# Performance work log

Hardware: AMD Instinct MI355X
Metric: run time of the kernel (lower is better)

## Reference

```python
import jax, jax.numpy as jnp
import numpy as np

D = 1024
H = 16
HD = D // H
FF = 4096
EPS = 1e-5


def setup_inputs() -> dict:
    key = jax.random.key(0)
    ks = jax.random.split(key, 12)
    s = lambda fan_in: 1.0 / np.sqrt(fan_in)
    return {
        "x": jax.random.normal(ks[0], (8, 1024, D), dtype=jnp.float32),
        "ln1_g": jnp.ones((D,), jnp.float32),
        "ln1_b": jnp.zeros((D,), jnp.float32),
        "ln2_g": jnp.ones((D,), jnp.float32),
        "ln2_b": jnp.zeros((D,), jnp.float32),
        "qkv_w": jax.random.uniform(ks[1], (3 * D, D), jnp.float32, -s(D), s(D)),
        "q_bias": jnp.zeros((D,), jnp.float32),
        "v_bias": jnp.zeros((D,), jnp.float32),
        "proj_w": jax.random.uniform(ks[2], (D, D), jnp.float32, -s(D), s(D)),
        "proj_b": jnp.zeros((D,), jnp.float32),
        "fc1_w": jax.random.uniform(ks[3], (FF, D), jnp.float32, -s(D), s(D)),
        "fc1_b": jnp.zeros((FF,), jnp.float32),
        "fc2_w": jax.random.uniform(ks[4], (D, FF), jnp.float32, -s(FF), s(FF)),
        "fc2_b": jnp.zeros((D,), jnp.float32),
    }


def _layernorm(x, g, b):
    mu = jnp.mean(x, axis=-1, keepdims=True)
    var = jnp.mean(jnp.square(x - mu), axis=-1, keepdims=True)
    return (x - mu) * jax.lax.rsqrt(var + EPS) * g + b


def reference(x, ln1_g, ln1_b, ln2_g, ln2_b, qkv_w, q_bias, v_bias,
              proj_w, proj_b, fc1_w, fc1_b, fc2_w, fc2_b):
    b, n, d = x.shape
    scale = HD ** (-0.5)
    # --- attention branch ---
    h = _layernorm(x, ln1_g, ln1_b)
    qkv_bias = jnp.concatenate([q_bias, jnp.zeros_like(v_bias), v_bias])
    qkv = h @ qkv_w.T + qkv_bias  # [b, n, 3d]
    qkv = qkv.reshape(b, n, 3, H, HD).transpose(2, 0, 3, 1, 4)  # [3, b, h, n, hd]
    q, k, v = qkv[0], qkv[1], qkv[2]
    attn = jnp.einsum("bhnd,bhmd->bhnm", q * scale, k)
    attn = jax.nn.softmax(attn, axis=-1)
    o = jnp.einsum("bhnm,bhmd->bhnd", attn, v)
    o = o.transpose(0, 2, 1, 3).reshape(b, n, d)
    x = x + (o @ proj_w.T + proj_b)
    # --- mlp branch ---
    h = _layernorm(x, ln2_g, ln2_b)
    h = jax.nn.gelu(h @ fc1_w.T + fc1_b, approximate=False)
    x = x + (h @ fc2_w.T + fc2_b)
    return x
```

## Files before the change

### kernel.cpp

```cpp
#include <hip/hip_runtime.h>
#include <hip/hip_bf16.h>


typedef __attribute__((ext_vector_type(8))) short short8;
typedef __attribute__((ext_vector_type(4))) float floatx4;

__device__ __forceinline__ unsigned short f2bf(float f) {
  union { __hip_bfloat16 h; unsigned short u; } cv;
  cv.h = __float2bfloat16(f);
  return cv.u;
}

__device__ __forceinline__ float fast_exp2(float x) {
  return __builtin_amdgcn_exp2f(x);
}

__device__ __forceinline__ void async_ld16(const void* g, void* l) {
  __builtin_amdgcn_global_load_lds(
      (const __attribute__((address_space(1))) unsigned int*)g,
      (__attribute__((address_space(3))) unsigned int*)l, 16, 0, 0);
}

#define VMCNT(n) asm volatile("s_waitcnt vmcnt(" #n ")" ::: "memory")

__global__ __launch_bounds__(256) void cvt_bf16(const float* __restrict__ in,
                                                unsigned short* __restrict__ out) {
  const long i = ((long)blockIdx.x * 256 + threadIdx.x) * 4;
  const float4 v = *(const float4*)(in + i);
  ushort4 o;
  o.x = f2bf(v.x); o.y = f2bf(v.y); o.z = f2bf(v.z); o.w = f2bf(v.w);
  *(ushort4*)(out + i) = o;
}

__global__ __launch_bounds__(256) void ln_bf16(const float* __restrict__ x,
                                               const float* __restrict__ g,
                                               const float* __restrict__ b,
                                               unsigned short* __restrict__ out) {
  const int row = blockIdx.x;
  const int tid = threadIdx.x;
  const float4 v = ((const float4*)(x + (long)row * 1024))[tid];
  float s = v.x + v.y + v.z + v.w;
  float ss = v.x * v.x + v.y * v.y + v.z * v.z + v.w * v.w;
#pragma unroll
  for (int off = 1; off < 64; off <<= 1) {
    s += __shfl_xor(s, off);
    ss += __shfl_xor(ss, off);
  }
  __shared__ float red[8];
  const int wave = tid >> 6, lane = tid & 63;
  if (lane == 0) { red[wave] = s; red[4 + wave] = ss; }
  __syncthreads();
  if (tid == 0) {
    red[0] = red[0] + red[1] + red[2] + red[3];
    red[4] = red[4] + red[5] + red[6] + red[7];
  }
  __syncthreads();
  const float mu = red[0] * (1.f / 1024.f);
  const float var = red[4] * (1.f / 1024.f) - mu * mu;
  const float rstd = rsqrtf(var + 1e-5f);
  const int c = tid * 4;
  ushort4 o;
  o.x = f2bf((v.x - mu) * rstd * g[c + 0] + b[c + 0]);
  o.y = f2bf((v.y - mu) * rstd * g[c + 1] + b[c + 1]);
  o.z = f2bf((v.z - mu) * rstd * g[c + 2] + b[c + 2]);
  o.w = f2bf((v.w - mu) * rstd * g[c + 3] + b[c + 3]);
  ((ushort4*)(out + (long)row * 1024))[tid] = o;
}

#define BM 128
#define BN 128

template <int MODE>
__global__ __launch_bounds__(256) void gemm_bt(
    const unsigned short* __restrict__ A, const unsigned short* __restrict__ B,
    int M, int N, int Kd,
    const float* __restrict__ b0, const float* __restrict__ b1,
    const float* __restrict__ resid,
    void* __restrict__ out0, void* __restrict__ out1, void* __restrict__ out2) {
  __shared__ unsigned short lA[3][BM * 32];
  __shared__ unsigned short lB[3][BN * 32];
  const int tid = threadIdx.x;
  const int wave = tid >> 6, lane = tid & 63;
  const int l16 = lane & 15, quad = lane >> 4;
  const int wr = wave >> 1, wc = wave & 1;
  const int bid = blockIdx.x;
  const int xcd = bid & 7;
  const int s = bid >> 3;
  const long m0 = (long)(xcd * 8 + (s & 7)) * BM;
  const long n0 = (long)(s >> 3) * BN;

  const int row = tid >> 2;
  const int kc = (tid & 3) ^ ((row >> 1) & 3);
  const unsigned short* aSrc = A + (m0 + row) * Kd + kc * 8;
  const unsigned short* bSrc = B + (n0 + row) * Kd + kc * 8;
  const int ldsOff0 = wave * 1024;
  const int ldsOff1 = wave * 1024 + 4096;

  floatx4 acc[4][4];
#pragma unroll
  for (int i = 0; i < 4; i++)
#pragma unroll
    for (int j = 0; j < 4; j++) acc[i][j] = (floatx4){0.f, 0.f, 0.f, 0.f};

#pragma unroll
  for (int bp = 0; bp < 2; bp++) {
    const int kk = bp * 32;
    async_ld16(aSrc + kk, (char*)&lA[bp][0] + ldsOff0);
    async_ld16(aSrc + 64 * Kd + kk, (char*)&lA[bp][0] + ldsOff1);
    async_ld16(bSrc + kk, (char*)&lB[bp][0] + ldsOff0);
    async_ld16(bSrc + 64 * Kd + kk, (char*)&lB[bp][0] + ldsOff1);
  }

  const int sw = ((l16 >> 1) & 3);

  int buf = 0;
  for (int k0 = 0; k0 < Kd; k0 += 32) {
    if (k0 + 32 < Kd) { VMCNT(4); } else { VMCNT(0); }
    __builtin_amdgcn_sched_barrier(0);
    __builtin_amdgcn_s_barrier();
    __builtin_amdgcn_sched_barrier(0);
    const int kn = k0 + 64;
    if (kn < Kd) {
      const int bp = (buf + 2 >= 3) ? buf - 1 : buf + 2;
      async_ld16(aSrc + kn, (char*)&lA[bp][0] + ldsOff0);
      async_ld16(aSrc + 64 * Kd + kn, (char*)&lA[bp][0] + ldsOff1);
      async_ld16(bSrc + kn, (char*)&lB[bp][0] + ldsOff0);
      async_ld16(bSrc + 64 * Kd + kn, (char*)&lB[bp][0] + ldsOff1);
    }
    short8 af[4], bfv[4];
#pragma unroll
    for (int mi = 0; mi < 4; mi++) {
      const int r = wr * 64 + mi * 16 + l16;
      af[mi] = *(const short8*)(&lA[buf][(r * 4 + (quad ^ sw)) * 8]);
    }
#pragma unroll
    for (int ni = 0; ni < 4; ni++) {
      const int r = wc * 64 + ni * 16 + l16;
      bfv[ni] = *(const short8*)(&lB[buf][(r * 4 + (quad ^ sw)) * 8]);
    }
#pragma unroll
    for (int mi = 0; mi < 4; mi++)
#pragma unroll
      for (int ni = 0; ni < 4; ni++)
        acc[mi][ni] = __builtin_amdgcn_mfma_f32_16x16x32_bf16(
            af[mi], bfv[ni], acc[mi][ni], 0, 0, 0);
    buf = (buf + 1 >= 3) ? 0 : buf + 1;
  }

#pragma unroll
  for (int mi = 0; mi < 4; mi++) {
    const long rbase = m0 + wr * 64 + mi * 16 + quad * 4;
#pragma unroll
    for (int ni = 0; ni < 4; ni++) {
      const long cg = n0 + wc * 64 + ni * 16 + l16;
      if (MODE == 0) {
        const int which = (int)(cg >> 10);
        const int col = (int)(cg & 1023);
        const int head = col >> 6, hd = col & 63;
        if (which == 2) {
          const int bidx = (int)(rbase >> 10);
          const int t = (int)(rbase & 1023);
          const long bh = bidx * 16 + head;
          const float bv = b1[col];
          ushort4 pk;
          pk.x = f2bf(acc[mi][ni][0] + bv);
          pk.y = f2bf(acc[mi][ni][1] + bv);
          pk.z = f2bf(acc[mi][ni][2] + bv);
          pk.w = f2bf(acc[mi][ni][3] + bv);
          *(ushort4*)((unsigned short*)out2 + (bh * 64 + hd) * 1024 + t) = pk;
        } else {
#pragma unroll
          for (int reg = 0; reg < 4; reg++) {
            const long rr = rbase + reg;
            const float val = acc[mi][ni][reg];
            const int bidx = (int)(rr >> 10), t = (int)(rr & 1023);
            const long bh = bidx * 16 + head;
            if (which == 0) {
              ((unsigned short*)out0)[(bh * 1024 + t) * 64 + hd] =
                  f2bf((val + b0[col]) * 0.1803368801111244f);
            } else {
              ((unsigned short*)out1)[(bh * 1024 + t) * 64 + hd] = f2bf(val);
            }
          }
        }
      } else {
#pragma unroll
        for (int reg = 0; reg < 4; reg++) {
          const long rr = rbase + reg;
          const float val = acc[mi][ni][reg];
          if (MODE == 1) {
            const long idx = rr * N + cg;
            ((float*)out0)[idx] = resid[idx] + val + b0[cg];
          } else {
            const float u = val + b0[cg];
            const float gl = 0.5f * u * (1.0f + erff(u * 0.70710678118f));
            ((unsigned short*)out0)[rr * N + cg] = f2bf(gl);
          }
        }
      }
    }
  }
  (void)M;
}

__global__ __launch_bounds__(256) void attn(const unsigned short* __restrict__ Q,
                                            const unsigned short* __restrict__ Kc,
                                            const unsigned short* __restrict__ Vt,
                                            unsigned short* __restrict__ O) {
  __shared__ unsigned short lK[2][2048];
  __shared__ unsigned short lV[2][2048];
  __shared__ float P[4][2][16][34];
  const int tid = threadIdx.x;
  const int wave = tid >> 6, lane = tid & 63;
  const int l16 = lane & 15, quad = lane >> 4;
  const int bid = blockIdx.x;
  const int xcd = bid & 7;
  const int sl = bid >> 3;
  const int bh = xcd * 16 + (sl & 15);
  const int q0 = (sl >> 4) * 128 + wave * 32;
  const unsigned short* Qb = Q + ((long)bh * 1024 + q0) * 64;
  const unsigned short* Kb = Kc + (long)bh * 65536;
  const unsigned short* Vb = Vt + (long)bh * 65536;

  short8 qf[2][2];
#pragma unroll
  for (int t = 0; t < 2; t++)
#pragma unroll
    for (int h = 0; h < 2; h++)
      qf[t][h] = *(const short8*)(Qb + (t * 16 + l16) * 64 + h * 32 + quad * 8);

  const int kr = tid >> 3;
  const int kc = (tid & 7) ^ (kr & 7);
  const unsigned short* kSrc = Kb + kr * 64 + kc * 8;
  const int vr = tid >> 2;
  const int vc = (tid & 3) ^ (vr & 3) ^ ((vr >> 2) & 3);
  const unsigned short* vSrc = Vb + vr * 1024 + vc * 8;

  floatx4 oacc[2][4];
#pragma unroll
  for (int t = 0; t < 2; t++)
#pragma unroll
    for (int u = 0; u < 4; u++) oacc[t][u] = (floatx4){0.f, 0.f, 0.f, 0.f};
  float lrun[2][4] = {{0.f, 0.f, 0.f, 0.f}, {0.f, 0.f, 0.f, 0.f}};

  async_ld16(kSrc, (char*)&lK[0][0] + wave * 1024);
  async_ld16(vSrc, (char*)&lV[0][0] + wave * 1024);

  const int vca = quad ^ (l16 & 3) ^ ((l16 >> 2) & 3);

  for (int ks = 0; ks < 1024; ks += 32) {
    const int buf = (ks >> 5) & 1;
    __syncthreads();
    const int kn = ks + 32;
    if (kn < 1024) {
      async_ld16(kSrc + kn * 64, (char*)&lK[buf ^ 1][0] + wave * 1024);
      async_ld16(vSrc + kn,      (char*)&lV[buf ^ 1][0] + wave * 1024);
    }
    short8 kf[2][2];
#pragma unroll
    for (int i = 0; i < 2; i++)
#pragma unroll
      for (int h = 0; h < 2; h++) {
        const int gr = (i * 16 + l16) * 8 + ((h * 4 + quad) ^ (l16 & 7));
        kf[i][h] = *(const short8*)(&lK[buf][gr * 8]);
      }
    floatx4 sres[2][2];
#pragma unroll
    for (int t = 0; t < 2; t++)
#pragma unroll
      for (int i = 0; i < 2; i++) {
        const floatx4 z = {0.f, 0.f, 0.f, 0.f};
        floatx4 a = __builtin_amdgcn_mfma_f32_16x16x32_bf16(qf[t][0], kf[i][0], z, 0, 0, 0);
        sres[t][i] = __builtin_amdgcn_mfma_f32_16x16x32_bf16(qf[t][1], kf[i][1], a, 0, 0, 0);
      }
#pragma unroll
    for (int t = 0; t < 2; t++)
#pragma unroll
      for (int r = 0; r < 4; r++) {
        const float p0 = fast_exp2(sres[t][0][r]);
        const float p1 = fast_exp2(sres[t][1][r]);
        lrun[t][r] += p0 + p1;
        P[wave][t][quad * 4 + r][l16] = p0;
        P[wave][t][quad * 4 + r][16 + l16] = p1;
      }
    short8 vf[4];
#pragma unroll
    for (int u = 0; u < 4; u++)
      vf[u] = *(const short8*)(&lV[buf][((u * 16 + l16) * 4 + vca) * 8]);
    short8 pf[2];
#pragma unroll
    for (int t = 0; t < 2; t++) {
      const float* pr = &P[wave][t][l16][quad * 8];
      const floatx4 pa = *(const floatx4*)pr;
      const floatx4 pb = *(const floatx4*)(pr + 4);
      pf[t][0] = (short)f2bf(pa[0]); pf[t][1] = (short)f2bf(pa[1]);
      pf[t][2] = (short)f2bf(pa[2]); pf[t][3] = (short)f2bf(pa[3]);
      pf[t][4] = (short)f2bf(pb[0]); pf[t][5] = (short)f2bf(pb[1]);
      pf[t][6] = (short)f2bf(pb[2]); pf[t][7] = (short)f2bf(pb[3]);
    }
#pragma unroll
    for (int t = 0; t < 2; t++)
#pragma unroll
      for (int u = 0; u < 4; u++)
        oacc[t][u] = __builtin_amdgcn_mfma_f32_16x16x32_bf16(pf[t], vf[u], oacc[t][u], 0, 0, 0);
  }

  const int b = bh >> 4, h = bh & 15;
#pragma unroll
  for (int t = 0; t < 2; t++) {
#pragma unroll
    for (int r = 0; r < 4; r++) {
      float lr = lrun[t][r];
      lr += __shfl_xor(lr, 1);
      lr += __shfl_xor(lr, 2);
      lr += __shfl_xor(lr, 4);
      lr += __shfl_xor(lr, 8);
      const float linv = 1.0f / lr;
#pragma unroll
      for (int u = 0; u < 4; u++) {
        O[((long)b * 1024 + q0 + t * 16 + quad * 4 + r) * 1024 + h * 64 + u * 16 + l16] =
            f2bf(oacc[t][u][r] * linv);
      }
    }
  }
}

extern "C" void kernel_launch(void* const* d_in, const int* in_sizes, int n_in,
                              void* d_out, int out_size, void* d_ws, size_t ws_size,
                              hipStream_t stream) {
  const float* x      = (const float*)d_in[0];
  const float* ln1_g  = (const float*)d_in[1];
  const float* ln1_b  = (const float*)d_in[2];
  const float* ln2_g  = (const float*)d_in[3];
  const float* ln2_b  = (const float*)d_in[4];
  const float* qkv_w  = (const float*)d_in[5];
  const float* q_bias = (const float*)d_in[6];
  const float* v_bias = (const float*)d_in[7];
  const float* proj_w = (const float*)d_in[8];
  const float* proj_b = (const float*)d_in[9];
  const float* fc1_w  = (const float*)d_in[10];
  const float* fc1_b  = (const float*)d_in[11];
  const float* fc2_w  = (const float*)d_in[12];
  const float* fc2_b  = (const float*)d_in[13];
  float* out = (float*)d_out;

  char* ws = (char*)d_ws;
  unsigned short* Wqkv  = (unsigned short*)(ws);
  unsigned short* Wproj = (unsigned short*)(ws + 6291456);
  unsigned short* Wfc1  = (unsigned short*)(ws + 8388608);
  unsigned short* Wfc2  = (unsigned short*)(ws + 16777216);
  float*          X1    = (float*)        (ws + 25165824);
  unsigned short* Hbuf  = (unsigned short*)(ws + 58720256);
  unsigned short* Qbuf  = (unsigned short*)(ws + 75497472);
  unsigned short* Kbuf  = (unsigned short*)(ws + 92274688);
  unsigned short* Vtbuf = (unsigned short*)(ws + 109051904);
  unsigned short* Obuf  = (unsigned short*)(ws + 125829120);
  unsigned short* ACT   = Qbuf;

  cvt_bf16<<<3072 * 1024 / 1024, 256, 0, stream>>>(qkv_w, Wqkv);
  cvt_bf16<<<1024 * 1024 / 1024, 256, 0, stream>>>(proj_w, Wproj);
  cvt_bf16<<<4096 * 1024 / 1024, 256, 0, stream>>>(fc1_w, Wfc1);
  cvt_bf16<<<4096 * 1024 / 1024, 256, 0, stream>>>(fc2_w, Wfc2);

  ln_bf16<<<8192, 256, 0, stream>>>(x, ln1_g, ln1_b, Hbuf);
  gemm_bt<0><<<24 * 64, 256, 0, stream>>>(Hbuf, Wqkv, 8192, 3072, 1024,
                                          q_bias, v_bias, nullptr,
                                          Qbuf, Kbuf, Vtbuf);
  attn<<<1024, 256, 0, stream>>>(Qbuf, Kbuf, Vtbuf, Obuf);
  gemm_bt<1><<<8 * 64, 256, 0, stream>>>(Obuf, Wproj, 8192, 1024, 1024,
                                         proj_b, nullptr, x,
                                         X1, nullptr, nullptr);
  ln_bf16<<<8192, 256, 0, stream>>>(X1, ln2_g, ln2_b, Hbuf);
  gemm_bt<2><<<32 * 64, 256, 0, stream>>>(Hbuf, Wfc1, 8192, 4096, 1024,
                                          fc1_b, nullptr, nullptr,
                                          ACT, nullptr, nullptr);
  gemm_bt<1><<<8 * 64, 256, 0, stream>>>(ACT, Wfc2, 8192, 1024, 4096,
                                         fc2_b, nullptr, X1,
                                         out, nullptr, nullptr);
  (void)in_sizes; (void)n_in; (void)out_size; (void)ws_size;
}
```

Baseline: 557.2 us.

## Use 256x128 tiles for QKV and FC1 GEMMs with shared epilogue helper

Adds a new GEMM kernel with 256x128 block tiles, where each wave computes 128x64 with an 8x4 MFMA accumulator grid, and a triple-buffered async LDS pipeline. The QKV and FC1 GEMMs switch to it, with grid sizes halved and an XCD-aware block mapping. Larger tiles raise arithmetic intensity and reuse of the B tile, cutting global and LDS traffic per FLOP. The cost is more accumulator registers (128 floats per lane) and LDS per block, which may lower occupancy. Epilogue logic moves into a shared template helper.

Result: slower. 623.5 us (+11.9%).

```diff
diff --git a/kernel.cpp b/kernel.cpp
--- a/kernel.cpp
+++ b/kernel.cpp
@@ -65,6 +65,59 @@
   o.z = f2bf((v.z - mu) * rstd * g[c + 2] + b[c + 2]);
   o.w = f2bf((v.w - mu) * rstd * g[c + 3] + b[c + 3]);
   ((ushort4*)(out + (long)row * 1024))[tid] = o;
+}
+
+template <int MODE>
+__device__ __forceinline__ void epi_tile(
+    long rbase, long cg, const floatx4& a, int N,
+    const float* __restrict__ b0, const float* __restrict__ b1,
+    const float* __restrict__ resid,
+    void* __restrict__ out0, void* __restrict__ out1, void* __restrict__ out2) {
+  if (MODE == 0) {
+    const int which = (int)(cg >> 10);
+    const int col = (int)(cg & 1023);
+    const int head = col >> 6, hd = col & 63;
+    if (which == 2) {
+      const int bidx = (int)(rbase >> 10);
+      const int t = (int)(rbase & 1023);
+      const long bh = bidx * 16 + head;
+      const float bv = b1[col];
+      ushort4 pk;
+      pk.x = f2bf(a[0] + bv);
+      pk.y = f2bf(a[1] + bv);
+      pk.z = f2bf(a[2] + bv);
+      pk.w = f2bf(a[3] + bv);
+      *(ushort4*)((unsigned short*)out2 + (bh * 64 + hd) * 1024 + t) = pk;
+    } else {
+#pragma unroll
+      for (int reg = 0; reg < 4; reg++) {
+        const long rr = rbase + reg;
+        const float val = a[reg];
+        const int bidx = (int)(rr >> 10), t = (int)(rr & 1023);
+        const long bh = bidx * 16 + head;
+        if (which == 0) {
+          ((unsigned short*)out0)[(bh * 1024 + t) * 64 + hd] =
+              f2bf((val + b0[col]) * 0.1803368801111244f);
+        } else {
+          ((unsigned short*)out1)[(bh * 1024 + t) * 64 + hd] = f2bf(val);
+        }
+      }
+    }
+  } else {
+#pragma unroll
+    for (int reg = 0; reg < 4; reg++) {
+      const long rr = rbase + reg;
+      const float val = a[reg];
+      if (MODE == 1) {
+        const long idx = rr * N + cg;
+        ((float*)out0)[idx] = resid[idx] + val + b0[cg];
+      } else {
+        const float u = val + b0[cg];
+        const float gl = 0.5f * u * (1.0f + erff(u * 0.70710678118f));
+        ((unsigned short*)out0)[rr * N + cg] = f2bf(gl);
+      }
+    }
+  }
 }
 
 #define BM 128
@@ -153,54 +206,105 @@
 #pragma unroll
     for (int ni = 0; ni < 4; ni++) {
       const long cg = n0 + wc * 64 + ni * 16 + l16;
-      if (MODE == 0) {
-        const int which = (int)(cg >> 10);
-        const int col = (int)(cg & 1023);
-        const int head = col >> 6, hd = col & 63;
-        if (which == 2) {
-          const int bidx = (int)(rbase >> 10);
-          const int t = (int)(rbase & 1023);
-          const long bh = bidx * 16 + head;
-          const float bv = b1[col];
-          ushort4 pk;
-          pk.x = f2bf(acc[mi][ni][0] + bv);
-          pk.y = f2bf(acc[mi][ni][1] + bv);
-          pk.z = f2bf(acc[mi][ni][2] + bv);
-          pk.w = f2bf(acc[mi][ni][3] + bv);
-          *(ushort4*)((unsigned short*)out2 + (bh * 64 + hd) * 1024 + t) = pk;
-        } else {
-#pragma unroll
-          for (int reg = 0; reg < 4; reg++) {
-            const long rr = rbase + reg;
-            const float val = acc[mi][ni][reg];
-            const int bidx = (int)(rr >> 10), t = (int)(rr & 1023);
-            const long bh = bidx * 16 + head;
-            if (which == 0) {
-              ((unsigned short*)out0)[(bh * 1024 + t) * 64 + hd] =
-                  f2bf((val + b0[col]) * 0.1803368801111244f);
-            } else {
-              ((unsigned short*)out1)[(bh * 1024 + t) * 64 + hd] = f2bf(val);
-            }
-          }
-        }
-      } else {
-#pragma unroll
-        for (int reg = 0; reg < 4; reg++) {
-          const long rr = rbase + reg;
-          const float val = acc[mi][ni][reg];
-          if (MODE == 1) {
-            const long idx = rr * N + cg;
-            ((float*)out0)[idx] = resid[idx] + val + b0[cg];
-          } else {
-            const float u = val + b0[cg];
-            const float gl = 0.5f * u * (1.0f + erff(u * 0.70710678118f));
-            ((unsigned short*)out0)[rr * N + cg] = f2bf(gl);
-          }
-        }
-      }
+      epi_tile<MODE>(rbase, cg, acc[mi][ni], N, b0, b1, resid,
+                     out0, out1, out2);
     }
   }
   (void)M;
+}
+
+template <int MODE>
+__global__ __launch_bounds__(256) void gemm_w(
+    const unsigned short* __restrict__ A, const unsigned short* __restrict__ B,
+    int M, int N, int Kd,
+    const float* __restrict__ b0, const float* __restrict__ b1,
+    const float* __restrict__ resid,
+    void* __restrict__ out0, void* __restrict__ out1, void* __restrict__ out2) {
+  __shared__ __align__(16) unsigned short lds3[3][12288];
+  const int tid = threadIdx.x;
+  const int wave = tid >> 6, lane = tid & 63;
+  const int l16 = lane & 15, quad = lane >> 4;
+  const int wr = wave >> 1, wc = wave & 1;
+  const int bid = blockIdx.x;
+  const int xcd = bid & 7;
+  const int s = bid >> 3;
+  const long m0 = (long)(xcd * 4 + (s & 3)) * 256;
+  const long n0 = (long)(s >> 2) * 128;
+
+  const int srow = tid >> 2;
+  const int skc = (tid & 3) ^ ((srow >> 1) & 3);
+  const unsigned short* aSrc = A + (m0 + srow) * Kd + skc * 8;
+  const unsigned short* bSrc = B + (n0 + srow) * Kd + skc * 8;
+  const int wvOff = wave * 1024;
+
+  floatx4 acc[8][4];
+#pragma unroll
+  for (int i = 0; i < 8; i++)
+#pragma unroll
+    for (int j = 0; j < 4; j++) acc[i][j] = (floatx4){0.f, 0.f, 0.f, 0.f};
+
+#define STAGE_W(bp, kk)                                                      \
+  do {                                                                       \
+    char* base_ = (char*)&lds3[bp][0];                                       \
+    async_ld16(aSrc + (kk), base_ + wvOff);                                  \
+    async_ld16(aSrc + (long)64 * Kd + (kk), base_ + 4096 + wvOff);           \
+    async_ld16(aSrc + (long)128 * Kd + (kk), base_ + 8192 + wvOff);          \
+    async_ld16(aSrc + (long)192 * Kd + (kk), base_ + 12288 + wvOff);         \
+    async_ld16(bSrc + (kk), base_ + 16384 + wvOff);                          \
+    async_ld16(bSrc + (long)64 * Kd + (kk), base_ + 20480 + wvOff);          \
+  } while (0)
+
+  STAGE_W(0, 0);
+  STAGE_W(1, 32);
+
+  const int sw = ((l16 >> 1) & 3);
+
+  int buf = 0;
+  for (int k0 = 0; k0 < Kd; k0 += 32) {
+    if (k0 + 32 < Kd) { VMCNT(6); } else { VMCNT(0); }
+    __builtin_amdgcn_sched_barrier(0);
+    __builtin_amdgcn_s_barrier();
+    __builtin_amdgcn_sched_barrier(0);
+    const int kn = k0 + 64;
+    if (kn < Kd) {
+      const int bp = (buf + 2 >= 3) ? buf - 1 : buf + 2;
+      STAGE_W(bp, kn);
+    }
+    const char* aBase = (const char*)&lds3[buf][0] + wr * 8192;
+    const char* bBase = (const char*)&lds3[buf][0] + 16384 + wc * 4096;
+    short8 af[8], bfv[4];
+#pragma unroll
+    for (int mi = 0; mi < 8; mi++) {
+      const int r63 = (mi & 3) * 16 + l16;
+      af[mi] = *(const short8*)(aBase + (mi >> 2) * 4096 +
+                                (r63 * 4 + (quad ^ sw)) * 16);
+    }
+#pragma unroll
+    for (int ni = 0; ni < 4; ni++) {
+      const int r63 = ni * 16 + l16;
+      bfv[ni] = *(const short8*)(bBase + (r63 * 4 + (quad ^ sw)) * 16);
+    }
+#pragma unroll
+    for (int mi = 0; mi < 8; mi++)
+#pragma unroll
+      for (int ni = 0; ni < 4; ni++)
+        acc[mi][ni] = __builtin_amdgcn_mfma_f32_16x16x32_bf16(
+            af[mi], bfv[ni], acc[mi][ni], 0, 0, 0);
+    buf = (buf + 1 >= 3) ? 0 : buf + 1;
+  }
+
+#pragma unroll
+  for (int mi = 0; mi < 8; mi++) {
+    const long rbase = m0 + wr * 128 + mi * 16 + quad * 4;
+#pragma unroll
+    for (int ni = 0; ni < 4; ni++) {
+      const long cg = n0 + wc * 64 + ni * 16 + l16;
+      epi_tile<MODE>(rbase, cg, acc[mi][ni], N, b0, b1, resid,
+                     out0, out1, out2);
+    }
+  }
+  (void)M;
+#undef STAGE_W
 }
 
 __global__ __launch_bounds__(256) void attn(const unsigned short* __restrict__ Q,
@@ -363,17 +467,17 @@
   cvt_bf16<<<4096 * 1024 / 1024, 256, 0, stream>>>(fc2_w, Wfc2);
 
   ln_bf16<<<8192, 256, 0, stream>>>(x, ln1_g, ln1_b, Hbuf);
-  gemm_bt<0><<<24 * 64, 256, 0, stream>>>(Hbuf, Wqkv, 8192, 3072, 1024,
-                                          q_bias, v_bias, nullptr,
-                                          Qbuf, Kbuf, Vtbuf);
+  gemm_w<0><<<768, 256, 0, stream>>>(Hbuf, Wqkv, 8192, 3072, 1024,
+                                     q_bias, v_bias, nullptr,
+                                     Qbuf, Kbuf, Vtbuf);
   attn<<<1024, 256, 0, stream>>>(Qbuf, Kbuf, Vtbuf, Obuf);
   gemm_bt<1><<<8 * 64, 256, 0, stream>>>(Obuf, Wproj, 8192, 1024, 1024,
                                          proj_b, nullptr, x,
                                          X1, nullptr, nullptr);
   ln_bf16<<<8192, 256, 0, stream>>>(X1, ln2_g, ln2_b, Hbuf);
-  gemm_bt<2><<<32 * 64, 256, 0, stream>>>(Hbuf, Wfc1, 8192, 4096, 1024,
-                                          fc1_b, nullptr, nullptr,
-                                          ACT, nullptr, nullptr);
+  gemm_w<2><<<1024, 256, 0, stream>>>(Hbuf, Wfc1, 8192, 4096, 1024,
+                                      fc1_b, nullptr, nullptr,
+                                      ACT, nullptr, nullptr);
   gemm_bt<1><<<8 * 64, 256, 0, stream>>>(ACT, Wfc2, 8192, 1024, 4096,
                                          fc2_b, nullptr, X1,
                                          out, nullptr, nullptr);
```
